# Kernel tuning notes

Measured on AMD Instinct MI355X. Metric: run time of the kernel, lower is better.

Reference implementation:

```python
import jax, jax.numpy as jnp
import numpy as np

N = 100000   # nodes
E = 1600000  # edges (avg degree 16)
DIM = 128    # feature dim
EPS = 1e-6
NEG_SLOPE = 0.2  # tf.nn.leaky_relu default alpha


def layernorm(x, g, b):
    m = jnp.mean(x, axis=-1, keepdims=True)
    v = jnp.mean(jnp.square(x - m), axis=-1, keepdims=True)
    return g * (x - m) * jax.lax.rsqrt(v + EPS) + b


def setup_inputs() -> dict:
    key = jax.random.key(0)
    ks = jax.random.split(key, 12)
    s = 1.0 / np.sqrt(DIM)
    return {
        "query": jax.random.normal(ks[0], (N, DIM), jnp.float32),
        "adj_val": jax.random.uniform(ks[1], (E,), jnp.float32),
        "w_W": jax.random.normal(ks[2], (DIM, DIM), jnp.float32) * s,
        "w_b": jnp.zeros((DIM,), jnp.float32),
        "w1_W": jax.random.normal(ks[3], (DIM, DIM), jnp.float32) * s,
        "w1_b": jnp.zeros((DIM,), jnp.float32),
        "w2_W": jax.random.normal(ks[4], (DIM, DIM), jnp.float32) * s,
        "w2_b": jnp.zeros((DIM,), jnp.float32),
        "ln1_g": jnp.ones((DIM,), jnp.float32),
        "ln1_b": jnp.zeros((DIM,), jnp.float32),
        "ln2_g": jnp.ones((DIM,), jnp.float32),
        "ln2_b": jnp.zeros((DIM,), jnp.float32),
        "adj_row": jnp.sort(jax.random.randint(ks[5], (E,), 0, N, jnp.int32)),
        "adj_col": jax.random.randint(ks[6], (E,), 0, N, jnp.int32),
    }


def reference(query, adj_val, w_W, w_b, w1_W, w1_b, w2_W, w2_b,
              ln1_g, ln1_b, ln2_g, ln2_b, adj_row, adj_col):
    q = layernorm(query, ln1_g, ln1_b)          # [N, D]
    k = q                                        # key is None -> key = query
    value = k @ w_W + w_b                        # [N, D]

    # per-node scalar scores (mean_sum=False branch); dropout in eval mode (identity)
    sum1 = jnp.tanh(jnp.sum(q @ w1_W + w1_b, axis=1))   # [N]
    sum2 = jnp.tanh(jnp.sum(k @ w2_W + w2_b, axis=1))   # [N]

    # sparse add of col-scaled and row-scaled adjacency, then leaky_relu
    logits = jax.nn.leaky_relu(
        adj_val * sum1[adj_row] + adj_val * sum2[adj_col], NEG_SLOPE)  # [E]

    # sparse row-wise softmax over nonzeros
    row_max = jax.ops.segment_max(logits, adj_row, num_segments=N)
    ex = jnp.exp(logits - row_max[adj_row])
    row_sum = jax.ops.segment_sum(ex, adj_row, num_segments=N)
    attn = ex / row_sum[adj_row]                 # [E]

    # spmm: out[i] = sum_e attn[e] * value[col[e]]
    out = jax.ops.segment_sum(attn[:, None] * value[adj_col], adj_row,
                              num_segments=N)    # [N, D]
    return layernorm(out, ln2_g, ln2_b)
```

## Files before the change

### kernel.cpp

```cpp
#include <hip/hip_runtime.h>
#include <hip/hip_bf16.h>

typedef __attribute__((ext_vector_type(8))) short short8;
typedef __attribute__((ext_vector_type(8))) unsigned short ushort8;
typedef __attribute__((ext_vector_type(4))) float f32x4;
typedef __attribute__((ext_vector_type(2))) float f32x2;
typedef __attribute__((ext_vector_type(4))) unsigned int uint4v;

#define DIM 128
#define EPS 1e-6f

__device__ __forceinline__ float wave_sum(float v){
  #pragma unroll
  for (int m = 32; m >= 1; m >>= 1) v += __shfl_xor(v, m);
  return v;
}

__global__ void setup_kernel(const float* __restrict__ w_W,
                             const float* __restrict__ w1_W, const float* __restrict__ w1_b,
                             const float* __restrict__ w2_W, const float* __restrict__ w2_b,
                             __hip_bfloat16* __restrict__ wt_bf,
                             float* __restrict__ u1, float* __restrict__ u2,
                             float* __restrict__ c12){
  const int b = blockIdx.x, tid = threadIdx.x;
  if (b == 0){
    if (tid < DIM){
      float s1 = 0.f, s2 = 0.f;
      for (int j = 0; j < DIM; ++j){ s1 += w1_W[tid*DIM + j]; s2 += w2_W[tid*DIM + j]; }
      u1[tid] = s1; u2[tid] = s2;
    }
    if (tid < 64){
      float c1 = w1_b[tid] + w1_b[tid + 64];
      float c2 = w2_b[tid] + w2_b[tid + 64];
      c1 = wave_sum(c1); c2 = wave_sum(c2);
      if (tid == 0){ c12[0] = c1; c12[1] = c2; }
    }
  } else {
    int idx = (b - 1) * 256 + tid;
    int j = idx >> 7, d = idx & 127;
    wt_bf[idx] = __float2bfloat16(w_W[d*DIM + j]);
  }
}

__launch_bounds__(256)
__global__ void node_kernel(const float* __restrict__ query,
                            const __hip_bfloat16* __restrict__ wt_bf,
                            const float* __restrict__ w_b,
                            const float* __restrict__ ln1_g, const float* __restrict__ ln1_b,
                            const float* __restrict__ u1, const float* __restrict__ u2,
                            const float* __restrict__ c12,
                            unsigned char* __restrict__ value_q,
                            float* __restrict__ sum1, float2* __restrict__ s2v, int N){
  __shared__ __hip_bfloat16 A[64][136];
  const int tid  = threadIdx.x;
  const int lane = tid & 63;
  const int w    = tid >> 6;
  const int q16  = lane >> 4;
  const int lq   = lane & 15;
  const int base = blockIdx.x * 64;

  float uu1[8], uu2[8], gg[8], bv[8];
  {
    const float* p1 = u1 + lq*8; const float* p2 = u2 + lq*8;
    const float* pg = ln1_g + lq*8; const float* pb = ln1_b + lq*8;
    #pragma unroll
    for (int j = 0; j < 8; ++j){ uu1[j]=p1[j]; uu2[j]=p2[j]; gg[j]=pg[j]; bv[j]=pb[j]; }
  }
  const float c1 = c12[0], c2 = c12[1];

  #pragma unroll
  for (int it = 0; it < 4; ++it){
    const int row = w*16 + it*4 + q16;
    const int n   = base + row;
    float x[8];
    if (n < N){
      const float* qp = query + (size_t)n*DIM + lq*8;
      #pragma unroll
      for (int j = 0; j < 8; ++j) x[j] = qp[j];
    } else {
      #pragma unroll
      for (int j = 0; j < 8; ++j) x[j] = 0.f;
    }
    float s = 0.f, s2 = 0.f;
    #pragma unroll
    for (int j = 0; j < 8; ++j){ s += x[j]; s2 += x[j]*x[j]; }
    #pragma unroll
    for (int m = 1; m <= 8; m <<= 1){ s += __shfl_xor(s, m); s2 += __shfl_xor(s2, m); }
    const float mean = s * (1.f/128.f);
    const float var  = s2 * (1.f/128.f) - mean*mean;
    const float rs   = rsqrtf(var + EPS);

    float p1 = 0.f, p2 = 0.f;
    unsigned pk[4];
    #pragma unroll
    for (int j = 0; j < 4; ++j){
      float n0 = gg[2*j]   * (x[2*j]   - mean) * rs + bv[2*j];
      float n1 = gg[2*j+1] * (x[2*j+1] - mean) * rs + bv[2*j+1];
      p1 += n0*uu1[2*j] + n1*uu1[2*j+1];
      p2 += n0*uu2[2*j] + n1*uu2[2*j+1];
      union { __hip_bfloat16 h; unsigned short u; } a_, b_;
      a_.h = __float2bfloat16(n0); b_.h = __float2bfloat16(n1);
      pk[j] = ((unsigned)b_.u << 16) | (unsigned)a_.u;
    }
    uint4v pv = { pk[0], pk[1], pk[2], pk[3] };
    *(uint4v*)&A[row][lq*8] = pv;
    #pragma unroll
    for (int m = 1; m <= 8; m <<= 1){ p1 += __shfl_xor(p1, m); p2 += __shfl_xor(p2, m); }
    if (lq == 0 && n < N){
      sum1[n]   = tanhf(p1 + c1);
      s2v[n].x  = tanhf(p2 + c2);
    }
  }
  __syncthreads();

  const int rh = (w & 1) * 32;
  const int ch = (w >> 1) * 64;
  short8 afr[2][4];
  #pragma unroll
  for (int m = 0; m < 2; ++m)
    #pragma unroll
    for (int ks = 0; ks < 4; ++ks)
      afr[m][ks] = *(const short8*)&A[rh + m*16 + lq][ks*32 + q16*8];
  __syncthreads();

  #pragma unroll
  for (int jj = 0; jj < 4; ++jj){
    const int colb = ch + jj*16;
    f32x4 acc[2];
    acc[0] = (f32x4){0.f,0.f,0.f,0.f};
    acc[1] = (f32x4){0.f,0.f,0.f,0.f};
    #pragma unroll
    for (int ks = 0; ks < 4; ++ks){
      short8 bfr = *(const short8*)(wt_bf + (size_t)(colb + lq)*DIM + ks*32 + q16*8);
      acc[0] = __builtin_amdgcn_mfma_f32_16x16x32_bf16(afr[0][ks], bfr, acc[0], 0, 0, 0);
      acc[1] = __builtin_amdgcn_mfma_f32_16x16x32_bf16(afr[1][ks], bfr, acc[1], 0, 0, 0);
    }
    const int col  = colb + lq;
    const float bias = w_b[col];
    #pragma unroll
    for (int m = 0; m < 2; ++m)
      #pragma unroll
      for (int i = 0; i < 4; ++i)
        A[rh + m*16 + q16*4 + i][col] = __float2bfloat16(acc[m][i] + bias);
  }
  __syncthreads();

  const int row = tid >> 2, seg = tid & 3;
  const int n = base + row;
  float vals[32];
  float amax = 0.f;
  const ushort8* ap = (const ushort8*)&A[row][seg*32];
  #pragma unroll
  for (int h = 0; h < 4; ++h){
    ushort8 vv = ap[h];
    #pragma unroll
    for (int j = 0; j < 8; ++j){
      float f = __uint_as_float((unsigned)vv[j] << 16);
      vals[h*8 + j] = f;
      amax = fmaxf(amax, fabsf(f));
    }
  }
  amax = fmaxf(amax, __shfl_xor(amax, 1));
  amax = fmaxf(amax, __shfl_xor(amax, 2));
  const float qs = amax > 0.f ? 127.f / amax : 0.f;
  if (n < N){
    if (seg == 0) s2v[n].y = amax * (1.f/127.f);
    unsigned dw[8];
    #pragma unroll
    for (int d = 0; d < 8; ++d){
      unsigned q0 = (unsigned)__float2int_rn(fmaf(vals[4*d+0], qs, 128.f));
      unsigned q1 = (unsigned)__float2int_rn(fmaf(vals[4*d+1], qs, 128.f));
      unsigned q2 = (unsigned)__float2int_rn(fmaf(vals[4*d+2], qs, 128.f));
      unsigned q3 = (unsigned)__float2int_rn(fmaf(vals[4*d+3], qs, 128.f));
      dw[d] = q0 | (q1 << 8) | (q2 << 16) | (q3 << 24);
    }
    uint4v* dst = (uint4v*)(value_q + (size_t)n*DIM + seg*32);
    dst[0] = (uint4v){dw[0], dw[1], dw[2], dw[3]};
    dst[1] = (uint4v){dw[4], dw[5], dw[6], dw[7]};
  }
}

__global__ void pack_kernel(const float* __restrict__ adj_val, const int* __restrict__ adj_row,
                            const int* __restrict__ adj_col,
                            const float* __restrict__ sum1, const float2* __restrict__ s2v,
                            float2* __restrict__ excol, int* __restrict__ row_ptr,
                            int N, int E){
  int e = blockIdx.x * 256 + threadIdx.x;
  if (e >= E) return;
  int r  = adj_row[e];
  int rp = (e > 0) ? adj_row[e-1] : -1;
  if (rp != r){
    for (int rr = rp + 1; rr <= r; ++rr) row_ptr[rr] = e;
  }
  if (e == E - 1){
    for (int rr = r + 1; rr <= N; ++rr) row_ptr[rr] = E;
  }
  float av = adj_val[e];
  int c = adj_col[e];
  float2 sv = s2v[c];
  float x = av * (sum1[r] + sv.x);
  float lg = x > 0.f ? x : 0.2f * x;
  excol[e] = make_float2(__expf(lg) * sv.y, __int_as_float(c << 7));
}

__launch_bounds__(256)
__global__ void edge_kernel(const float2* __restrict__ excol, const int* __restrict__ row_ptr,
                            const unsigned char* __restrict__ value_q,
                            const float* __restrict__ ln2_g, const float* __restrict__ ln2_b,
                            float* __restrict__ out, int N){
  const int lane = threadIdx.x & 63;
  const int r = blockIdx.x * 4 + (threadIdx.x >> 6);
  if (r >= N) return;
  const int e0 = row_ptr[r], e1 = row_ptr[r+1];
  const int q  = lane >> 4;
  const int lq = lane & 15;
  const unsigned char* vbase = value_q + lq*8;

  f32x2 acc2[4];
  #pragma unroll
  for (int j = 0; j < 4; ++j) acc2[j] = (f32x2){0.f, 0.f};
  float sumw = 0.f;

  for (int eb = e0 + q; eb < e1; eb += 16){
    #pragma unroll
    for (int t = 0; t < 4; ++t){
      const int e = eb + t*4;
      float2 ecv = (e < e1) ? excol[e] : make_float2(0.f, __int_as_float(0));
      const float wsc = ecv.x;
      const unsigned voff = (unsigned)__float_as_int(ecv.y);
      uint2 v = *(const uint2*)(vbase + voff);
      sumw += wsc;
      f32x2 w2 = { wsc, wsc };
      f32x2 p0 = { (float)( v.x        & 0xff), (float)((v.x >>  8) & 0xff) };
      f32x2 p1 = { (float)((v.x >> 16) & 0xff), (float)( v.x >> 24)         };
      f32x2 p2 = { (float)( v.y        & 0xff), (float)((v.y >>  8) & 0xff) };
      f32x2 p3 = { (float)((v.y >> 16) & 0xff), (float)( v.y >> 24)         };
      acc2[0] += w2 * p0;
      acc2[1] += w2 * p1;
      acc2[2] += w2 * p2;
      acc2[3] += w2 * p3;
    }
  }

  #pragma unroll
  for (int j = 0; j < 4; ++j){
    acc2[j].x += __shfl_xor(acc2[j].x, 16); acc2[j].y += __shfl_xor(acc2[j].y, 16);
    acc2[j].x += __shfl_xor(acc2[j].x, 32); acc2[j].y += __shfl_xor(acc2[j].y, 32);
  }
  sumw += __shfl_xor(sumw, 16);
  sumw += __shfl_xor(sumw, 32);

  const float bias = 128.f * sumw;
  #pragma unroll
  for (int j = 0; j < 4; ++j){ acc2[j].x -= bias; acc2[j].y -= bias; }

  float sx = 0.f, sxx = 0.f;
  #pragma unroll
  for (int j = 0; j < 4; ++j){
    sx  += acc2[j].x + acc2[j].y;
    sxx += acc2[j].x*acc2[j].x + acc2[j].y*acc2[j].y;
  }
  #pragma unroll
  for (int m = 1; m <= 8; m <<= 1){ sx += __shfl_xor(sx, m); sxx += __shfl_xor(sxx, m); }
  const float mean = sx * (1.f/128.f);
  const float var  = sxx * (1.f/128.f) - mean*mean;
  const float rs   = rsqrtf(var + EPS);

  if (q == 0){
    float4 g0 = ((const float4*)ln2_g)[lq*2], g1 = ((const float4*)ln2_g)[lq*2+1];
    float4 b0 = ((const float4*)ln2_b)[lq*2], b1 = ((const float4*)ln2_b)[lq*2+1];
    float4 o0, o1;
    o0.x = g0.x*(acc2[0].x-mean)*rs + b0.x; o0.y = g0.y*(acc2[0].y-mean)*rs + b0.y;
    o0.z = g0.z*(acc2[1].x-mean)*rs + b0.z; o0.w = g0.w*(acc2[1].y-mean)*rs + b0.w;
    o1.x = g1.x*(acc2[2].x-mean)*rs + b1.x; o1.y = g1.y*(acc2[2].y-mean)*rs + b1.y;
    o1.z = g1.z*(acc2[3].x-mean)*rs + b1.z; o1.w = g1.w*(acc2[3].y-mean)*rs + b1.w;
    float4* op = (float4*)(out + (size_t)r*DIM + lq*8);
    op[0] = o0; op[1] = o1;
  }
}

extern "C" void kernel_launch(void* const* d_in, const int* in_sizes, int n_in,
                              void* d_out, int out_size, void* d_ws, size_t ws_size,
                              hipStream_t stream){
  const float* query   = (const float*)d_in[0];
  const float* adj_val = (const float*)d_in[1];
  const float* w_W     = (const float*)d_in[2];
  const float* w_b     = (const float*)d_in[3];
  const float* w1_W    = (const float*)d_in[4];
  const float* w1_b    = (const float*)d_in[5];
  const float* w2_W    = (const float*)d_in[6];
  const float* w2_b    = (const float*)d_in[7];
  const float* ln1_g   = (const float*)d_in[8];
  const float* ln1_b   = (const float*)d_in[9];
  const float* ln2_g   = (const float*)d_in[10];
  const float* ln2_b   = (const float*)d_in[11];
  const int*   adj_row = (const int*)d_in[12];
  const int*   adj_col = (const int*)d_in[13];

  const int N = in_sizes[0] / DIM;
  const int E = in_sizes[1];

  char* ws = (char*)d_ws;
  size_t off = 0;
  unsigned char* value_q = (unsigned char*)(ws + off); off += (size_t)N * DIM;
  float* sum1   = (float*)(ws + off); off += (size_t)N * 4;
  float2* s2v   = (float2*)(ws + off); off += (size_t)N * 8;
  int* row_ptr  = (int*)(ws + off);   off += (size_t)(N + 2) * 4;
  float* u1     = (float*)(ws + off); off += DIM * 4;
  float* u2     = (float*)(ws + off); off += DIM * 4;
  float* c12    = (float*)(ws + off); off += 2 * 4;
  off = (off + 63) & ~(size_t)63;
  __hip_bfloat16* wt_bf = (__hip_bfloat16*)(ws + off); off += DIM * DIM * 2;
  off = (off + 63) & ~(size_t)63;
  float2* excol = (float2*)(ws + off);

  setup_kernel<<<65, 256, 0, stream>>>(w_W, w1_W, w1_b, w2_W, w2_b, wt_bf, u1, u2, c12);
  node_kernel<<<(N + 63) / 64, 256, 0, stream>>>(query, wt_bf, w_b, ln1_g, ln1_b,
                                                 u1, u2, c12, value_q, sum1, s2v, N);
  pack_kernel<<<(E + 255) / 256, 256, 0, stream>>>(adj_val, adj_row, adj_col,
                                                   sum1, s2v, excol, row_ptr, N, E);
  edge_kernel<<<(N + 3) / 4, 256, 0, stream>>>(excol, row_ptr, value_q,
                                               ln2_g, ln2_b, (float*)d_out, N);
}
```

Before: 106.4 us.

## Process two rows per wave in edge kernel and drop redundant bias correction

The edge kernel now gives each row a half-wave of 32 lanes (two edge groups) instead of a full wave, so each block covers 8 rows. The main loop becomes an unpredicated 8-edge body with a separate guarded tail. The per-row weight-sum bias subtraction is removed, since a uniform shift per row cancels inside the following layernorm. The setup kernel's weight row sums are split across 256 threads with float4 loads, and the node kernel loads query with float4. The cost is a longer serial edge loop per lane group on high-degree rows.

```diff
diff --git a/kernel.cpp b/kernel.cpp
--- a/kernel.cpp
+++ b/kernel.cpp
@@ -24,11 +24,19 @@
                              float* __restrict__ c12){
   const int b = blockIdx.x, tid = threadIdx.x;
   if (b == 0){
-    if (tid < DIM){
-      float s1 = 0.f, s2 = 0.f;
-      for (int j = 0; j < DIM; ++j){ s1 += w1_W[tid*DIM + j]; s2 += w2_W[tid*DIM + j]; }
-      u1[tid] = s1; u2[tid] = s2;
-    }
+    __shared__ float p1s[256], p2s[256];
+    const int d = tid & 127, half = tid >> 7;
+    const float4* w1p = (const float4*)(w1_W + d*DIM + half*64);
+    const float4* w2p = (const float4*)(w2_W + d*DIM + half*64);
+    float s1 = 0.f, s2 = 0.f;
+    #pragma unroll 4
+    for (int j = 0; j < 16; ++j){
+      float4 a = w1p[j]; s1 += (a.x + a.y) + (a.z + a.w);
+      float4 c = w2p[j]; s2 += (c.x + c.y) + (c.z + c.w);
+    }
+    p1s[tid] = s1; p2s[tid] = s2;
+    __syncthreads();
+    if (tid < 128){ u1[tid] = p1s[tid] + p1s[tid+128]; u2[tid] = p2s[tid] + p2s[tid+128]; }
     if (tid < 64){
       float c1 = w1_b[tid] + w1_b[tid + 64];
       float c2 = w2_b[tid] + w2_b[tid + 64];
@@ -74,9 +82,10 @@
     const int n   = base + row;
     float x[8];
     if (n < N){
-      const float* qp = query + (size_t)n*DIM + lq*8;
-      #pragma unroll
-      for (int j = 0; j < 8; ++j) x[j] = qp[j];
+      const float4* qp = (const float4*)(query + (size_t)n*DIM + lq*8);
+      float4 a = qp[0], b = qp[1];
+      x[0]=a.x; x[1]=a.y; x[2]=a.z; x[3]=a.w;
+      x[4]=b.x; x[5]=b.y; x[6]=b.z; x[7]=b.w;
     } else {
       #pragma unroll
       for (int j = 0; j < 8; ++j) x[j] = 0.f;
@@ -209,27 +218,28 @@
                             const float* __restrict__ ln2_g, const float* __restrict__ ln2_b,
                             float* __restrict__ out, int N){
   const int lane = threadIdx.x & 63;
-  const int r = blockIdx.x * 4 + (threadIdx.x >> 6);
+  const int half = lane >> 5;
+  const int ll   = lane & 31;
+  const int q2   = ll >> 4;
+  const int lq   = ll & 15;
+  const int r = blockIdx.x * 8 + (threadIdx.x >> 6) * 2 + half;
   if (r >= N) return;
-  const int e0 = row_ptr[r], e1 = row_ptr[r+1];
-  const int q  = lane >> 4;
-  const int lq = lane & 15;
+  const int2 rp = *(const int2*)(row_ptr + r);
+  const int e0 = rp.x, e1 = rp.y;
   const unsigned char* vbase = value_q + lq*8;
 
   f32x2 acc2[4];
   #pragma unroll
   for (int j = 0; j < 4; ++j) acc2[j] = (f32x2){0.f, 0.f};
-  float sumw = 0.f;
-
-  for (int eb = e0 + q; eb < e1; eb += 16){
+
+  int sb = e0;
+  for (; sb + 8 <= e1; sb += 8){
     #pragma unroll
     for (int t = 0; t < 4; ++t){
-      const int e = eb + t*4;
-      float2 ecv = (e < e1) ? excol[e] : make_float2(0.f, __int_as_float(0));
+      float2 ecv = excol[sb + q2 + t*2];
       const float wsc = ecv.x;
       const unsigned voff = (unsigned)__float_as_int(ecv.y);
       uint2 v = *(const uint2*)(vbase + voff);
-      sumw += wsc;
       f32x2 w2 = { wsc, wsc };
       f32x2 p0 = { (float)( v.x        & 0xff), (float)((v.x >>  8) & 0xff) };
       f32x2 p1 = { (float)((v.x >> 16) & 0xff), (float)( v.x >> 24)         };
@@ -241,18 +251,31 @@
       acc2[3] += w2 * p3;
     }
   }
+  if (sb < e1){
+    #pragma unroll
+    for (int t = 0; t < 4; ++t){
+      const int e = sb + q2 + t*2;
+      float2 ecv = (e < e1) ? excol[e] : make_float2(0.f, 0.f);
+      const float wsc = ecv.x;
+      const unsigned voff = (unsigned)__float_as_int(ecv.y);
+      uint2 v = *(const uint2*)(vbase + voff);
+      f32x2 w2 = { wsc, wsc };
+      f32x2 p0 = { (float)( v.x        & 0xff), (float)((v.x >>  8) & 0xff) };
+      f32x2 p1 = { (float)((v.x >> 16) & 0xff), (float)( v.x >> 24)         };
+      f32x2 p2 = { (float)( v.y        & 0xff), (float)((v.y >>  8) & 0xff) };
+      f32x2 p3 = { (float)((v.y >> 16) & 0xff), (float)( v.y >> 24)         };
+      acc2[0] += w2 * p0;
+      acc2[1] += w2 * p1;
+      acc2[2] += w2 * p2;
+      acc2[3] += w2 * p3;
+    }
+  }
 
   #pragma unroll
   for (int j = 0; j < 4; ++j){
-    acc2[j].x += __shfl_xor(acc2[j].x, 16); acc2[j].y += __shfl_xor(acc2[j].y, 16);
-    acc2[j].x += __shfl_xor(acc2[j].x, 32); acc2[j].y += __shfl_xor(acc2[j].y, 32);
-  }
-  sumw += __shfl_xor(sumw, 16);
-  sumw += __shfl_xor(sumw, 32);
-
-  const float bias = 128.f * sumw;
-  #pragma unroll
-  for (int j = 0; j < 4; ++j){ acc2[j].x -= bias; acc2[j].y -= bias; }
+    acc2[j].x += __shfl_xor(acc2[j].x, 16);
+    acc2[j].y += __shfl_xor(acc2[j].y, 16);
+  }
 
   float sx = 0.f, sxx = 0.f;
   #pragma unroll
@@ -266,7 +289,7 @@
   const float var  = sxx * (1.f/128.f) - mean*mean;
   const float rs   = rsqrtf(var + EPS);
 
-  if (q == 0){
+  if (q2 == 0){
     float4 g0 = ((const float4*)ln2_g)[lq*2], g1 = ((const float4*)ln2_g)[lq*2+1];
     float4 b0 = ((const float4*)ln2_b)[lq*2], b1 = ((const float4*)ln2_b)[lq*2+1];
     float4 o0, o1;
@@ -319,6 +342,6 @@
                                                  u1, u2, c12, value_q, sum1, s2v, N);
   pack_kernel<<<(E + 255) / 256, 256, 0, stream>>>(adj_val, adj_row, adj_col,
                                                    sum1, s2v, excol, row_ptr, N, E);
-  edge_kernel<<<(N + 3) / 4, 256, 0, stream>>>(excol, row_ptr, value_q,
+  edge_kernel<<<(N + 7) / 8, 256, 0, stream>>>(excol, row_ptr, value_q,
                                                ln2_g, ln2_b, (float*)d_out, N);
 }
```

Measured after the change: 93.13 us. -12.5%, faster.
